# Optimization experiments

Hardware: AMD Instinct MI355X
Metric: run time of the kernel (lower is better)

Reference implementation:

```python
import jax, jax.numpy as jnp
import numpy as np

EPS = 1e-10
NUM_RELATION = 4
N_NODES = 50000
N_EDGES = 800000
D_IN = 128
D_H = 256


def rgc_layer(x, src, dst, rel, rel_w, rel_b, loop_w, loop_b):
    # torchdrug RelationalGraphConv: scatter-mean per (node, relation), then
    # linear over concatenated per-relation features + self-loop linear + relu.
    N, d = x.shape
    msg = x[src]                                      # [E, d] gather
    idx = dst * NUM_RELATION + rel                    # [E] bucket per (node, relation)
    num_seg = N * NUM_RELATION
    agg = jax.ops.segment_sum(msg, idx, num_segments=num_seg)            # [N*R, d]
    cnt = jax.ops.segment_sum(jnp.ones((msg.shape[0], 1), x.dtype), idx,
                              num_segments=num_seg)                       # [N*R, 1]
    update = (agg / (cnt + EPS)).reshape(N, NUM_RELATION * d)            # [N, R*d]
    out = update @ rel_w + rel_b + x @ loop_w + loop_b                   # [N, d_out]
    return jax.nn.relu(out)


def highway(x, hp_w, hp_b, ht_w, ht_b):
    proj = jax.nn.relu(x @ hp_w + hp_b)
    gate = jax.nn.sigmoid(x @ ht_w + ht_b)
    return gate * proj + (1.0 - gate) * x


def setup_inputs() -> dict:
    key = jax.random.key(0)
    ks = jax.random.split(key, 16)
    s = 0.02
    inp = {
        "x": jax.random.normal(ks[0], (N_NODES, D_IN), dtype=jnp.float32),
        "src": jax.random.randint(ks[1], (N_EDGES,), 0, N_NODES, dtype=jnp.int32),
        "dst": jax.random.randint(ks[2], (N_EDGES,), 0, N_NODES, dtype=jnp.int32),
        "rel": jax.random.randint(ks[3], (N_EDGES,), 0, NUM_RELATION, dtype=jnp.int32),
        # layer 1: RGC(128->256) + Highway(256)
        "rel_w1": jax.random.normal(ks[4], (NUM_RELATION * D_IN, D_H), dtype=jnp.float32) * s,
        "rel_b1": jnp.zeros((D_H,), jnp.float32),
        "loop_w1": jax.random.normal(ks[5], (D_IN, D_H), dtype=jnp.float32) * s,
        "loop_b1": jnp.zeros((D_H,), jnp.float32),
        "hp_w1": jax.random.normal(ks[6], (D_H, D_H), dtype=jnp.float32) * s,
        "hp_b1": jnp.zeros((D_H,), jnp.float32),
        "ht_w1": jax.random.normal(ks[7], (D_H, D_H), dtype=jnp.float32) * s,
        "ht_b1": jnp.full((D_H,), -2.0, jnp.float32),  # transform.bias.data.fill_(-2.0)
        # layer 2: RGC(256->256) + Highway(256)
        "rel_w2": jax.random.normal(ks[8], (NUM_RELATION * D_H, D_H), dtype=jnp.float32) * s,
        "rel_b2": jnp.zeros((D_H,), jnp.float32),
        "loop_w2": jax.random.normal(ks[9], (D_H, D_H), dtype=jnp.float32) * s,
        "loop_b2": jnp.zeros((D_H,), jnp.float32),
        "hp_w2": jax.random.normal(ks[10], (D_H, D_H), dtype=jnp.float32) * s,
        "hp_b2": jnp.zeros((D_H,), jnp.float32),
        "ht_w2": jax.random.normal(ks[11], (D_H, D_H), dtype=jnp.float32) * s,
        "ht_b2": jnp.full((D_H,), -2.0, jnp.float32),
    }
    return inp


def reference(x, src, dst, rel,
              rel_w1, rel_b1, loop_w1, loop_b1, hp_w1, hp_b1, ht_w1, ht_b1,
              rel_w2, rel_b2, loop_w2, loop_b2, hp_w2, hp_b2, ht_w2, ht_b2):
    h = rgc_layer(x, src, dst, rel, rel_w1, rel_b1, loop_w1, loop_b1)
    h = highway(h, hp_w1, hp_b1, ht_w1, ht_b1)
    h = rgc_layer(h, src, dst, rel, rel_w2, rel_b2, loop_w2, loop_b2)
    h = highway(h, hp_w2, hp_b2, ht_w2, ht_b2)
    return h  # node_feature, shape [N, 256]
```

## Files before the change

### kernel.cpp

```cpp
#include <hip/hip_runtime.h>

typedef __bf16 bf16_t;
typedef __bf16 bf16x8 __attribute__((ext_vector_type(8)));
typedef __bf16 bf16x4 __attribute__((ext_vector_type(4)));
typedef float f32x4 __attribute__((ext_vector_type(4)));

#define BM 128
#define BN 128
#define BK 64

__device__ __forceinline__ void gload_lds16(const void* g, void* s) {
    __builtin_amdgcn_global_load_lds(
        (const __attribute__((address_space(1))) unsigned int*)g,
        (__attribute__((address_space(3))) unsigned int*)s, 16, 0, 0);
}

__global__ __launch_bounds__(256) void gemm_k(
    const bf16_t* __restrict__ A, int lda, int M,
    const bf16_t* __restrict__ Bt, int K,
    const float* __restrict__ bias, int relu_flag,
    bf16_t* __restrict__ outb, int ldo, int ocol,
    int NTM, int NTN)
{
    __shared__ __align__(16) bf16_t As[BM * BK];
    __shared__ __align__(16) bf16_t Bs[BN * BK];

    const int L    = blockIdx.x;
    const int xcd  = L & 7;
    const int rest = L >> 3;
    const int nt   = rest % NTN;
    const int sup  = rest / NTN;
    const int mt   = sup * 8 + xcd;
    if (mt >= NTM) return;
    const int m0 = mt * BM;
    const int n0 = nt * BN;

    const int tid  = threadIdx.x;
    const int wave = tid >> 6, lane = tid & 63;
    const int wr   = wave >> 1, wc = wave & 1;
    const int lm   = lane & 15, quad = lane >> 4;

    const bf16_t* ag[4];
    const bf16_t* bg[4];
    #pragma unroll
    for (int j = 0; j < 4; j++) {
        int c    = wave * 256 + j * 64 + lane;
        int row  = c >> 3;
        int cc   = (c & 7) ^ (row & 7);
        int col  = cc << 3;
        int gm   = m0 + row; if (gm >= M) gm = M - 1;
        ag[j] = A  + (size_t)gm * lda + col;
        bg[j] = Bt + (size_t)(n0 + row) * K + col;
    }

    f32x4 acc[4][4] = {};

    for (int k0 = 0; k0 < K; k0 += BK) {
        __syncthreads();
        #pragma unroll
        for (int j = 0; j < 4; j++)
            gload_lds16(ag[j] + k0, As + (size_t)(wave * 256 + j * 64) * 8);
        #pragma unroll
        for (int j = 0; j < 4; j++)
            gload_lds16(bg[j] + k0, Bs + (size_t)(wave * 256 + j * 64) * 8);
        __syncthreads();

        #pragma unroll
        for (int h = 0; h < 2; h++) {
            bf16x8 af[4], bfr[4];
            #pragma unroll
            for (int i = 0; i < 4; i++) {
                int r = wr * 64 + i * 16 + lm;
                af[i] = *(const bf16x8*)&As[(size_t)(r * 8 + ((h * 4 + quad) ^ (r & 7))) * 8];
            }
            #pragma unroll
            for (int i = 0; i < 4; i++) {
                int r = wc * 64 + i * 16 + lm;
                bfr[i] = *(const bf16x8*)&Bs[(size_t)(r * 8 + ((h * 4 + quad) ^ (r & 7))) * 8];
            }
            #pragma unroll
            for (int mi = 0; mi < 4; mi++)
                #pragma unroll
                for (int ni = 0; ni < 4; ni++)
                    acc[mi][ni] = __builtin_amdgcn_mfma_f32_16x16x32_bf16(
                        af[mi], bfr[ni], acc[mi][ni], 0, 0, 0);
        }
    }

    #pragma unroll
    for (int mi = 0; mi < 4; mi++) {
        #pragma unroll
        for (int ni = 0; ni < 4; ni++) {
            int col = n0 + wc * 64 + ni * 16 + lm;
            float b = bias[col];
            #pragma unroll
            for (int r = 0; r < 4; r++) {
                int row = m0 + wr * 64 + mi * 16 + quad * 4 + r;
                if (row < M) {
                    float v = acc[mi][ni][r] + b;
                    if (relu_flag) v = fmaxf(v, 0.f);
                    outb[(size_t)row * ldo + ocol + col] = (bf16_t)v;
                }
            }
        }
    }
}

__global__ void count_k(const int* __restrict__ dst, const int* __restrict__ rel,
                        int* __restrict__ cnt, int E)
{
    int e = blockIdx.x * blockDim.x + threadIdx.x;
    if (e < E) atomicAdd(&cnt[dst[e] * 4 + rel[e]], 1);
}

__global__ void scan_partial(const int* __restrict__ cnt, int* __restrict__ offs,
                             int* __restrict__ chunkSums, int NSEG)
{
    __shared__ int sh[256];
    int t = threadIdx.x;
    int idx = blockIdx.x * 256 + t;
    int v = (idx < NSEG) ? cnt[idx] : 0;
    sh[t] = v;
    __syncthreads();
    for (int d = 1; d < 256; d <<= 1) {
        int add = (t >= d) ? sh[t - d] : 0;
        __syncthreads();
        sh[t] += add;
        __syncthreads();
    }
    if (idx < NSEG) offs[idx] = sh[t] - v;
    if (t == 255) chunkSums[blockIdx.x] = sh[t];
}

__global__ void scan_chunks(int* __restrict__ chunkSums, int NCHUNK)
{
    __shared__ int sh[1024];
    int t = threadIdx.x;
    int v = (t < NCHUNK) ? chunkSums[t] : 0;
    sh[t] = v;
    __syncthreads();
    for (int d = 1; d < 1024; d <<= 1) {
        int add = (t >= d) ? sh[t - d] : 0;
        __syncthreads();
        sh[t] += add;
        __syncthreads();
    }
    if (t < NCHUNK) chunkSums[t] = sh[t] - v;
}

__global__ void scan_add(int* __restrict__ offs, const int* __restrict__ chunkSums,
                         int* __restrict__ cursor, int NSEG)
{
    int idx = blockIdx.x * 256 + threadIdx.x;
    if (idx < NSEG) {
        int o = offs[idx] + chunkSums[blockIdx.x];
        offs[idx] = o;
        cursor[idx] = o;
    }
}

__global__ void fill_k(const int* __restrict__ src, const int* __restrict__ dst,
                       const int* __restrict__ rel,
                       int* __restrict__ cursor, int* __restrict__ eidx, int E)
{
    int e = blockIdx.x * blockDim.x + threadIdx.x;
    if (e < E) {
        int seg = dst[e] * 4 + rel[e];
        int pos = atomicAdd(&cursor[seg], 1);
        eidx[pos] = src[e];
    }
}

__global__ void seg_mean256(const int* __restrict__ offs, const int* __restrict__ cnt,
                            const int* __restrict__ eidx,
                            const bf16_t* __restrict__ xb, int ldx,
                            bf16_t* __restrict__ Aout, int lda, int NSEG)
{
    int wv = (blockIdx.x << 2) + (threadIdx.x >> 6);
    if (wv >= NSEG) return;
    int lane = threadIdx.x & 63;
    int c = lane << 2;
    int start = offs[wv];
    int n = cnt[wv];
    f32x4 acc = {};
    int i = 0;
    for (; i + 4 <= n; i += 4) {
        int s0 = eidx[start + i + 0];
        int s1 = eidx[start + i + 1];
        int s2 = eidx[start + i + 2];
        int s3 = eidx[start + i + 3];
        bf16x4 v0 = *(const bf16x4*)(xb + (size_t)s0 * ldx + c);
        bf16x4 v1 = *(const bf16x4*)(xb + (size_t)s1 * ldx + c);
        bf16x4 v2 = *(const bf16x4*)(xb + (size_t)s2 * ldx + c);
        bf16x4 v3 = *(const bf16x4*)(xb + (size_t)s3 * ldx + c);
        #pragma unroll
        for (int j = 0; j < 4; j++)
            acc[j] += ((float)v0[j] + (float)v1[j]) + ((float)v2[j] + (float)v3[j]);
    }
    for (; i < n; i++) {
        int s = eidx[start + i];
        bf16x4 v = *(const bf16x4*)(xb + (size_t)s * ldx + c);
        #pragma unroll
        for (int j = 0; j < 4; j++) acc[j] += (float)v[j];
    }
    float inv = 1.0f / ((float)n + 1e-10f);
    int node = wv >> 2, r = wv & 3;
    bf16x4 o;
    o[0] = (bf16_t)(acc[0] * inv);
    o[1] = (bf16_t)(acc[1] * inv);
    o[2] = (bf16_t)(acc[2] * inv);
    o[3] = (bf16_t)(acc[3] * inv);
    *(bf16x4*)(Aout + (size_t)node * lda + r * 256 + c) = o;
}

__global__ void seg_mean128(const int* __restrict__ offs, const int* __restrict__ cnt,
                            const int* __restrict__ eidx,
                            const bf16_t* __restrict__ xb, int ldx,
                            bf16_t* __restrict__ Aout, int lda, int NSEG)
{
    int wv = (blockIdx.x << 2) + (threadIdx.x >> 6);
    if (wv >= NSEG) return;
    int lane = threadIdx.x & 63;
    int half = lane >> 5;
    int c = (lane & 31) << 2;
    int start = offs[wv];
    int n = cnt[wv];
    f32x4 acc = {};
    int i = 0;
    for (; i + 4 <= n; i += 4) {
        int s0 = eidx[start + i + half];
        int s1 = eidx[start + i + 2 + half];
        bf16x4 v0 = *(const bf16x4*)(xb + (size_t)s0 * ldx + c);
        bf16x4 v1 = *(const bf16x4*)(xb + (size_t)s1 * ldx + c);
        #pragma unroll
        for (int j = 0; j < 4; j++) acc[j] += (float)v0[j] + (float)v1[j];
    }
    for (; i + 2 <= n; i += 2) {
        int s = eidx[start + i + half];
        bf16x4 v = *(const bf16x4*)(xb + (size_t)s * ldx + c);
        #pragma unroll
        for (int j = 0; j < 4; j++) acc[j] += (float)v[j];
    }
    if (i < n && half == 0) {
        int s = eidx[start + i];
        bf16x4 v = *(const bf16x4*)(xb + (size_t)s * ldx + c);
        #pragma unroll
        for (int j = 0; j < 4; j++) acc[j] += (float)v[j];
    }
    #pragma unroll
    for (int j = 0; j < 4; j++) acc[j] += __shfl_xor(acc[j], 32, 64);
    if (half == 0) {
        float inv = 1.0f / ((float)n + 1e-10f);
        int node = wv >> 2, r = wv & 3;
        bf16x4 o;
        o[0] = (bf16_t)(acc[0] * inv);
        o[1] = (bf16_t)(acc[1] * inv);
        o[2] = (bf16_t)(acc[2] * inv);
        o[3] = (bf16_t)(acc[3] * inv);
        *(bf16x4*)(Aout + (size_t)node * lda + r * 128 + c) = o;
    }
}

__global__ void convert_x_k(const float* __restrict__ x, bf16_t* __restrict__ A1, int N)
{
    int t = blockIdx.x * blockDim.x + threadIdx.x;
    if (t >= N * 32) return;
    int row = t >> 5;
    int c = (t & 31) << 2;
    f32x4 v = *(const f32x4*)(x + (size_t)row * 128 + c);
    bf16x4 o;
    o[0] = (bf16_t)v[0]; o[1] = (bf16_t)v[1]; o[2] = (bf16_t)v[2]; o[3] = (bf16_t)v[3];
    *(bf16x4*)(A1 + (size_t)row * 640 + 512 + c) = o;
}

__global__ void transpose_w(const float* __restrict__ W, bf16_t* __restrict__ Wt,
                            int K, int ldk, int k0, int n0)
{
    int t = blockIdx.x * blockDim.x + threadIdx.x;
    if (t >= K * 256) return;
    int k = t >> 8, n = t & 255;
    Wt[(size_t)(n0 + n) * ldk + k0 + k] = (bf16_t)W[(size_t)k * 256 + n];
}

__global__ void prep_bias(const float* rb1, const float* lb1,
                          const float* rb2, const float* lb2,
                          const float* hpb1, const float* htb1,
                          const float* hpb2, const float* htb2,
                          float* bR1, float* bR2, float* bH1, float* bH2)
{
    int t = threadIdx.x;
    bR1[t] = rb1[t] + lb1[t];
    bR2[t] = rb2[t] + lb2[t];
    bH1[t] = hpb1[t]; bH1[256 + t] = htb1[t];
    bH2[t] = hpb2[t]; bH2[256 + t] = htb2[t];
}

__global__ void highway_k(const bf16_t* __restrict__ PG, const bf16_t* __restrict__ h,
                          int N, bf16_t* __restrict__ outb, int ldo, int ocol,
                          float* __restrict__ outf)
{
    int t = blockIdx.x * blockDim.x + threadIdx.x;
    if (t >= N * 64) return;
    int row = t >> 6;
    int c = (t & 63) << 2;
    size_t ip = (size_t)row * 512 + c;
    bf16x4 p = *(const bf16x4*)(PG + ip);
    bf16x4 g = *(const bf16x4*)(PG + ip + 256);
    bf16x4 hv = *(const bf16x4*)(h + (size_t)row * 256 + c);
    bf16x4 ob;
    f32x4 of;
    #pragma unroll
    for (int j = 0; j < 4; j++) {
        float gg = 1.0f / (1.0f + __expf(-(float)g[j]));
        float pp = fmaxf((float)p[j], 0.f);
        float v = gg * pp + (1.0f - gg) * (float)hv[j];
        ob[j] = (bf16_t)v;
        of[j] = v;
    }
    if (outb) *(bf16x4*)(outb + (size_t)row * ldo + ocol + c) = ob;
    if (outf) *(f32x4*)(outf + (size_t)row * 256 + c) = of;
}

extern "C" void kernel_launch(void* const* d_in, const int* in_sizes, int n_in,
                              void* d_out, int out_size, void* d_ws, size_t ws_size,
                              hipStream_t stream)
{
    const float* x       = (const float*)d_in[0];
    const int*   src     = (const int*)d_in[1];
    const int*   dst     = (const int*)d_in[2];
    const int*   rel     = (const int*)d_in[3];
    const float* rel_w1  = (const float*)d_in[4];
    const float* rel_b1  = (const float*)d_in[5];
    const float* loop_w1 = (const float*)d_in[6];
    const float* loop_b1 = (const float*)d_in[7];
    const float* hp_w1   = (const float*)d_in[8];
    const float* hp_b1   = (const float*)d_in[9];
    const float* ht_w1   = (const float*)d_in[10];
    const float* ht_b1   = (const float*)d_in[11];
    const float* rel_w2  = (const float*)d_in[12];
    const float* rel_b2  = (const float*)d_in[13];
    const float* loop_w2 = (const float*)d_in[14];
    const float* loop_b2 = (const float*)d_in[15];
    const float* hp_w2   = (const float*)d_in[16];
    const float* hp_b2   = (const float*)d_in[17];
    const float* ht_w2   = (const float*)d_in[18];
    const float* ht_b2   = (const float*)d_in[19];

    const int N = in_sizes[0] / 128;
    const int E = in_sizes[1];
    const int NSEG = N * 4;
    const int NCHUNK = (NSEG + 255) / 256;
    float* out = (float*)d_out;

    char* ws = (char*)d_ws;
    size_t off = 0;
    auto alloc = [&](size_t bytes) {
        void* p = ws + off;
        off += (bytes + 255) & ~(size_t)255;
        return p;
    };
    int*    cnt    = (int*)alloc((size_t)NSEG * 4);
    int*    offs   = (int*)alloc((size_t)NSEG * 4);
    int*    cursor = (int*)alloc((size_t)NSEG * 4);
    int*    chunkS = (int*)alloc(4096);
    int*    eidx   = (int*)alloc((size_t)E * 4);
    bf16_t* A1     = (bf16_t*)alloc((size_t)N * 640 * 2);
    bf16_t* A2     = (bf16_t*)alloc((size_t)N * 1280 * 2);
    bf16_t* h      = (bf16_t*)alloc((size_t)N * 256 * 2);
    bf16_t* W1t    = (bf16_t*)alloc((size_t)256 * 640 * 2);
    bf16_t* W2t    = (bf16_t*)alloc((size_t)256 * 1280 * 2);
    bf16_t* Wh1t   = (bf16_t*)alloc((size_t)512 * 256 * 2);
    bf16_t* Wh2t   = (bf16_t*)alloc((size_t)512 * 256 * 2);
    float*  bR1    = (float*)alloc(256 * 4);
    float*  bR2    = (float*)alloc(256 * 4);
    float*  bH1    = (float*)alloc(512 * 4);
    float*  bH2    = (float*)alloc(512 * 4);
    bf16_t* PG     = A1;

    dim3 blk(256);
    const int NTM = (N + BM - 1) / BM;
    const int supers = (NTM + 7) / 8;
    const int gridRGC = supers * 8 * 2;
    const int gridHW  = supers * 8 * 4;

    transpose_w<<<dim3(512), blk, 0, stream>>>(rel_w1, W1t, 512, 640, 0, 0);
    transpose_w<<<dim3(128), blk, 0, stream>>>(loop_w1, W1t, 128, 640, 512, 0);
    transpose_w<<<dim3(1024), blk, 0, stream>>>(rel_w2, W2t, 1024, 1280, 0, 0);
    transpose_w<<<dim3(256), blk, 0, stream>>>(loop_w2, W2t, 256, 1280, 1024, 0);
    transpose_w<<<dim3(256), blk, 0, stream>>>(hp_w1, Wh1t, 256, 256, 0, 0);
    transpose_w<<<dim3(256), blk, 0, stream>>>(ht_w1, Wh1t, 256, 256, 0, 256);
    transpose_w<<<dim3(256), blk, 0, stream>>>(hp_w2, Wh2t, 256, 256, 0, 0);
    transpose_w<<<dim3(256), blk, 0, stream>>>(ht_w2, Wh2t, 256, 256, 0, 256);
    prep_bias<<<dim3(1), blk, 0, stream>>>(rel_b1, loop_b1, rel_b2, loop_b2,
                                           hp_b1, ht_b1, hp_b2, ht_b2,
                                           bR1, bR2, bH1, bH2);
    convert_x_k<<<dim3((N * 32 + 255) / 256), blk, 0, stream>>>(x, A1, N);

    hipMemsetAsync(cnt, 0, (size_t)NSEG * 4, stream);
    count_k<<<dim3((E + 255) / 256), blk, 0, stream>>>(dst, rel, cnt, E);
    scan_partial<<<dim3(NCHUNK), blk, 0, stream>>>(cnt, offs, chunkS, NSEG);
    scan_chunks<<<dim3(1), dim3(1024), 0, stream>>>(chunkS, NCHUNK);
    scan_add<<<dim3(NCHUNK), blk, 0, stream>>>(offs, chunkS, cursor, NSEG);
    fill_k<<<dim3((E + 255) / 256), blk, 0, stream>>>(src, dst, rel, cursor, eidx, E);

    seg_mean128<<<dim3((NSEG + 3) / 4), blk, 0, stream>>>(offs, cnt, eidx,
                                                          A1 + 512, 640, A1, 640, NSEG);
    gemm_k<<<dim3(gridRGC), blk, 0, stream>>>(A1, 640, N, W1t, 640,
                                              bR1, 1, h, 256, 0, NTM, 2);
    gemm_k<<<dim3(gridHW), blk, 0, stream>>>(h, 256, N, Wh1t, 256,
                                             bH1, 0, PG, 512, 0, NTM, 4);
    highway_k<<<dim3((N * 64 + 255) / 256), blk, 0, stream>>>(PG, h, N,
                                                              A2, 1280, 1024, nullptr);

    seg_mean256<<<dim3((NSEG + 3) / 4), blk, 0, stream>>>(offs, cnt, eidx,
                                                          A2 + 1024, 1280, A2, 1280, NSEG);
    gemm_k<<<dim3(gridRGC), blk, 0, stream>>>(A2, 1280, N, W2t, 1280,
                                              bR2, 1, h, 256, 0, NTM, 2);
    gemm_k<<<dim3(gridHW), blk, 0, stream>>>(h, 256, N, Wh2t, 256,
                                             bH2, 0, PG, 512, 0, NTM, 4);
    highway_k<<<dim3((N * 64 + 255) / 256), blk, 0, stream>>>(PG, h, N,
                                                              nullptr, 0, 0, out);
}
```

Before: 582.1 us.

## Fuse highway gate/proj GEMM with highway epilogue and widen segment-mean loads

```diff
diff --git a/kernel.cpp b/kernel.cpp
--- a/kernel.cpp
+++ b/kernel.cpp
@@ -106,6 +106,108 @@
     }
 }
 
+__global__ __launch_bounds__(256) void gemm_hw(
+    const bf16_t* __restrict__ A, int M,
+    const bf16_t* __restrict__ Bt,
+    const float* __restrict__ bias,
+    bf16_t* __restrict__ outb, int ldo, int ocol,
+    float* __restrict__ outf, int NTM)
+{
+    const int K = 256;
+    __shared__ __align__(16) bf16_t As[128 * 64];
+    __shared__ __align__(16) bf16_t Bs[2 * 128 * 64];
+
+    const int L    = blockIdx.x;
+    const int xcd  = L & 7;
+    const int rest = L >> 3;
+    const int nt   = rest % 2;
+    const int sup  = rest / 2;
+    const int mt   = sup * 8 + xcd;
+    if (mt >= NTM) return;
+    const int m0 = mt * 128;
+
+    const int tid  = threadIdx.x;
+    const int wave = tid >> 6, lane = tid & 63;
+    const int wr   = wave >> 1, wc = wave & 1;
+    const int lm   = lane & 15, quad = lane >> 4;
+
+    const bf16_t* ag[4];
+    const bf16_t* bg[4];
+    #pragma unroll
+    for (int j = 0; j < 4; j++) {
+        int c    = wave * 256 + j * 64 + lane;
+        int row  = c >> 3;
+        int cc   = (c & 7) ^ (row & 7);
+        int col  = cc << 3;
+        int gm   = m0 + row; if (gm >= M) gm = M - 1;
+        ag[j] = A  + (size_t)gm * 256 + col;
+        bg[j] = Bt + (size_t)(nt * 128 + row) * 256 + col;
+    }
+
+    f32x4 acc[4][8] = {};
+
+    for (int k0 = 0; k0 < K; k0 += 64) {
+        __syncthreads();
+        #pragma unroll
+        for (int j = 0; j < 4; j++)
+            gload_lds16(ag[j] + k0, As + (size_t)(wave * 256 + j * 64) * 8);
+        #pragma unroll
+        for (int j = 0; j < 4; j++)
+            gload_lds16(bg[j] + k0, Bs + (size_t)(wave * 256 + j * 64) * 8);
+        #pragma unroll
+        for (int j = 0; j < 4; j++)
+            gload_lds16(bg[j] + 65536 + k0,
+                        Bs + (size_t)(8192 + wave * 256 + j * 64) * 8);
+        __syncthreads();
+
+        #pragma unroll
+        for (int h = 0; h < 2; h++) {
+            bf16x8 af[4], bfr[8];
+            #pragma unroll
+            for (int i = 0; i < 4; i++) {
+                int r = wr * 64 + i * 16 + lm;
+                af[i] = *(const bf16x8*)&As[(size_t)(r * 8 + ((h * 4 + quad) ^ (r & 7))) * 8];
+            }
+            #pragma unroll
+            for (int i = 0; i < 8; i++) {
+                int strip = i >> 2;
+                int r = wc * 64 + (i & 3) * 16 + lm;
+                bfr[i] = *(const bf16x8*)&Bs[(size_t)(strip * 8192 + r * 8 +
+                                                      ((h * 4 + quad) ^ (r & 7))) * 8];
+            }
+            #pragma unroll
+            for (int mi = 0; mi < 4; mi++)
+                #pragma unroll
+                for (int ni = 0; ni < 8; ni++)
+                    acc[mi][ni] = __builtin_amdgcn_mfma_f32_16x16x32_bf16(
+                        af[mi], bfr[ni], acc[mi][ni], 0, 0, 0);
+        }
+    }
+
+    #pragma unroll
+    for (int mi = 0; mi < 4; mi++) {
+        #pragma unroll
+        for (int ni = 0; ni < 4; ni++) {
+            int cP = nt * 128 + wc * 64 + ni * 16 + lm;
+            float bp = bias[cP];
+            float bgc = bias[256 + cP];
+            #pragma unroll
+            for (int r = 0; r < 4; r++) {
+                int row = m0 + wr * 64 + mi * 16 + quad * 4 + r;
+                if (row < M) {
+                    float p = acc[mi][ni][r] + bp;
+                    float g = acc[mi][ni + 4][r] + bgc;
+                    float s = 1.0f / (1.0f + __expf(-g));
+                    float hv = (float)A[(size_t)row * 256 + cP];
+                    float v = s * fmaxf(p, 0.f) + (1.0f - s) * hv;
+                    if (outf) outf[(size_t)row * 256 + cP] = v;
+                    else      outb[(size_t)row * ldo + ocol + cP] = (bf16_t)v;
+                }
+            }
+        }
+    }
+}
+
 __global__ void count_k(const int* __restrict__ dst, const int* __restrict__ rel,
                         int* __restrict__ cnt, int E)
 {
@@ -179,38 +281,47 @@
     int wv = (blockIdx.x << 2) + (threadIdx.x >> 6);
     if (wv >= NSEG) return;
     int lane = threadIdx.x & 63;
-    int c = lane << 2;
+    int half = lane >> 5;
+    int c = (lane & 31) << 3;
     int start = offs[wv];
     int n = cnt[wv];
-    f32x4 acc = {};
+    float acc[8] = {};
     int i = 0;
-    for (; i + 4 <= n; i += 4) {
-        int s0 = eidx[start + i + 0];
-        int s1 = eidx[start + i + 1];
-        int s2 = eidx[start + i + 2];
-        int s3 = eidx[start + i + 3];
-        bf16x4 v0 = *(const bf16x4*)(xb + (size_t)s0 * ldx + c);
-        bf16x4 v1 = *(const bf16x4*)(xb + (size_t)s1 * ldx + c);
-        bf16x4 v2 = *(const bf16x4*)(xb + (size_t)s2 * ldx + c);
-        bf16x4 v3 = *(const bf16x4*)(xb + (size_t)s3 * ldx + c);
-        #pragma unroll
-        for (int j = 0; j < 4; j++)
+    for (; i + 8 <= n; i += 8) {
+        int s0 = eidx[start + i + 0 + half];
+        int s1 = eidx[start + i + 2 + half];
+        int s2 = eidx[start + i + 4 + half];
+        int s3 = eidx[start + i + 6 + half];
+        bf16x8 v0 = *(const bf16x8*)(xb + (size_t)s0 * ldx + c);
+        bf16x8 v1 = *(const bf16x8*)(xb + (size_t)s1 * ldx + c);
+        bf16x8 v2 = *(const bf16x8*)(xb + (size_t)s2 * ldx + c);
+        bf16x8 v3 = *(const bf16x8*)(xb + (size_t)s3 * ldx + c);
+        #pragma unroll
+        for (int j = 0; j < 8; j++)
             acc[j] += ((float)v0[j] + (float)v1[j]) + ((float)v2[j] + (float)v3[j]);
     }
-    for (; i < n; i++) {
+    for (; i + 2 <= n; i += 2) {
+        int s = eidx[start + i + half];
+        bf16x8 v = *(const bf16x8*)(xb + (size_t)s * ldx + c);
+        #pragma unroll
+        for (int j = 0; j < 8; j++) acc[j] += (float)v[j];
+    }
+    if (i < n && half == 0) {
         int s = eidx[start + i];
-        bf16x4 v = *(const bf16x4*)(xb + (size_t)s * ldx + c);
-        #pragma unroll
-        for (int j = 0; j < 4; j++) acc[j] += (float)v[j];
-    }
-    float inv = 1.0f / ((float)n + 1e-10f);
-    int node = wv >> 2, r = wv & 3;
-    bf16x4 o;
-    o[0] = (bf16_t)(acc[0] * inv);
-    o[1] = (bf16_t)(acc[1] * inv);
-    o[2] = (bf16_t)(acc[2] * inv);
-    o[3] = (bf16_t)(acc[3] * inv);
-    *(bf16x4*)(Aout + (size_t)node * lda + r * 256 + c) = o;
+        bf16x8 v = *(const bf16x8*)(xb + (size_t)s * ldx + c);
+        #pragma unroll
+        for (int j = 0; j < 8; j++) acc[j] += (float)v[j];
+    }
+    #pragma unroll
+    for (int j = 0; j < 8; j++) acc[j] += __shfl_xor(acc[j], 32, 64);
+    if (half == 0) {
+        float inv = 1.0f / ((float)n + 1e-10f);
+        int node = wv >> 2, r = wv & 3;
+        bf16x8 o;
+        #pragma unroll
+        for (int j = 0; j < 8; j++) o[j] = (bf16_t)(acc[j] * inv);
+        *(bf16x8*)(Aout + (size_t)node * lda + r * 256 + c) = o;
+    }
 }
 
 __global__ void seg_mean128(const int* __restrict__ offs, const int* __restrict__ cnt,
@@ -221,43 +332,44 @@
     int wv = (blockIdx.x << 2) + (threadIdx.x >> 6);
     if (wv >= NSEG) return;
     int lane = threadIdx.x & 63;
-    int half = lane >> 5;
-    int c = (lane & 31) << 2;
+    int q = lane >> 4;
+    int c = (lane & 15) << 3;
     int start = offs[wv];
     int n = cnt[wv];
-    f32x4 acc = {};
+    float acc[8] = {};
     int i = 0;
+    for (; i + 8 <= n; i += 8) {
+        int s0 = eidx[start + i + q];
+        int s1 = eidx[start + i + 4 + q];
+        bf16x8 v0 = *(const bf16x8*)(xb + (size_t)s0 * ldx + c);
+        bf16x8 v1 = *(const bf16x8*)(xb + (size_t)s1 * ldx + c);
+        #pragma unroll
+        for (int j = 0; j < 8; j++) acc[j] += (float)v0[j] + (float)v1[j];
+    }
     for (; i + 4 <= n; i += 4) {
-        int s0 = eidx[start + i + half];
-        int s1 = eidx[start + i + 2 + half];
-        bf16x4 v0 = *(const bf16x4*)(xb + (size_t)s0 * ldx + c);
-        bf16x4 v1 = *(const bf16x4*)(xb + (size_t)s1 * ldx + c);
-        #pragma unroll
-        for (int j = 0; j < 4; j++) acc[j] += (float)v0[j] + (float)v1[j];
-    }
-    for (; i + 2 <= n; i += 2) {
-        int s = eidx[start + i + half];
-        bf16x4 v = *(const bf16x4*)(xb + (size_t)s * ldx + c);
-        #pragma unroll
-        for (int j = 0; j < 4; j++) acc[j] += (float)v[j];
-    }
-    if (i < n && half == 0) {
-        int s = eidx[start + i];
-        bf16x4 v = *(const bf16x4*)(xb + (size_t)s * ldx + c);
-        #pragma unroll
-        for (int j = 0; j < 4; j++) acc[j] += (float)v[j];
+        int s = eidx[start + i + q];
+        bf16x8 v = *(const bf16x8*)(xb + (size_t)s * ldx + c);
+        #pragma unroll
+        for (int j = 0; j < 8; j++) acc[j] += (float)v[j];
+    }
+    if (q < n - i) {
+        int s = eidx[start + i + q];
+        bf16x8 v = *(const bf16x8*)(xb + (size_t)s * ldx + c);
+        #pragma unroll
+        for (int j = 0; j < 8; j++) acc[j] += (float)v[j];
     }
     #pragma unroll
-    for (int j = 0; j < 4; j++) acc[j] += __shfl_xor(acc[j], 32, 64);
-    if (half == 0) {
+    for (int j = 0; j < 8; j++) {
+        acc[j] += __shfl_xor(acc[j], 16, 64);
+        acc[j] += __shfl_xor(acc[j], 32, 64);
+    }
+    if (lane < 16) {
         float inv = 1.0f / ((float)n + 1e-10f);
         int node = wv >> 2, r = wv & 3;
-        bf16x4 o;
-        o[0] = (bf16_t)(acc[0] * inv);
-        o[1] = (bf16_t)(acc[1] * inv);
-        o[2] = (bf16_t)(acc[2] * inv);
-        o[3] = (bf16_t)(acc[3] * inv);
-        *(bf16x4*)(Aout + (size_t)node * lda + r * 128 + c) = o;
+        bf16x8 o;
+        #pragma unroll
+        for (int j = 0; j < 8; j++) o[j] = (bf16_t)(acc[j] * inv);
+        *(bf16x8*)(Aout + (size_t)node * lda + r * 128 + c) = o;
     }
 }
 
@@ -293,32 +405,6 @@
     bR2[t] = rb2[t] + lb2[t];
     bH1[t] = hpb1[t]; bH1[256 + t] = htb1[t];
     bH2[t] = hpb2[t]; bH2[256 + t] = htb2[t];
-}
-
-__global__ void highway_k(const bf16_t* __restrict__ PG, const bf16_t* __restrict__ h,
-                          int N, bf16_t* __restrict__ outb, int ldo, int ocol,
-                          float* __restrict__ outf)
-{
-    int t = blockIdx.x * blockDim.x + threadIdx.x;
-    if (t >= N * 64) return;
-    int row = t >> 6;
-    int c = (t & 63) << 2;
-    size_t ip = (size_t)row * 512 + c;
-    bf16x4 p = *(const bf16x4*)(PG + ip);
-    bf16x4 g = *(const bf16x4*)(PG + ip + 256);
-    bf16x4 hv = *(const bf16x4*)(h + (size_t)row * 256 + c);
-    bf16x4 ob;
-    f32x4 of;
-    #pragma unroll
-    for (int j = 0; j < 4; j++) {
-        float gg = 1.0f / (1.0f + __expf(-(float)g[j]));
-        float pp = fmaxf((float)p[j], 0.f);
-        float v = gg * pp + (1.0f - gg) * (float)hv[j];
-        ob[j] = (bf16_t)v;
-        of[j] = v;
-    }
-    if (outb) *(bf16x4*)(outb + (size_t)row * ldo + ocol + c) = ob;
-    if (outf) *(f32x4*)(outf + (size_t)row * 256 + c) = of;
 }
 
 extern "C" void kernel_launch(void* const* d_in, const int* in_sizes, int n_in,
@@ -375,13 +461,12 @@
     float*  bR2    = (float*)alloc(256 * 4);
     float*  bH1    = (float*)alloc(512 * 4);
     float*  bH2    = (float*)alloc(512 * 4);
-    bf16_t* PG     = A1;
 
     dim3 blk(256);
     const int NTM = (N + BM - 1) / BM;
     const int supers = (NTM + 7) / 8;
     const int gridRGC = supers * 8 * 2;
-    const int gridHW  = supers * 8 * 4;
+    const int gridHW  = supers * 8 * 2;
 
     transpose_w<<<dim3(512), blk, 0, stream>>>(rel_w1, W1t, 512, 640, 0, 0);
     transpose_w<<<dim3(128), blk, 0, stream>>>(loop_w1, W1t, 128, 640, 512, 0);
@@ -407,17 +492,13 @@
                                                           A1 + 512, 640, A1, 640, NSEG);
     gemm_k<<<dim3(gridRGC), blk, 0, stream>>>(A1, 640, N, W1t, 640,
                                               bR1, 1, h, 256, 0, NTM, 2);
-    gemm_k<<<dim3(gridHW), blk, 0, stream>>>(h, 256, N, Wh1t, 256,
-                                             bH1, 0, PG, 512, 0, NTM, 4);
-    highway_k<<<dim3((N * 64 + 255) / 256), blk, 0, stream>>>(PG, h, N,
-                                                              A2, 1280, 1024, nullptr);
+    gemm_hw<<<dim3(gridHW), blk, 0, stream>>>(h, N, Wh1t, bH1,
+                                              A2, 1280, 1024, nullptr, NTM);
 
     seg_mean256<<<dim3((NSEG + 3) / 4), blk, 0, stream>>>(offs, cnt, eidx,
                                                           A2 + 1024, 1280, A2, 1280, NSEG);
     gemm_k<<<dim3(gridRGC), blk, 0, stream>>>(A2, 1280, N, W2t, 1280,
                                               bR2, 1, h, 256, 0, NTM, 2);
-    gemm_k<<<dim3(gridHW), blk, 0, stream>>>(h, 256, N, Wh2t, 256,
-                                             bH2, 0, PG, 512, 0, NTM, 4);
-    highway_k<<<dim3((N * 64 + 255) / 256), blk, 0, stream>>>(PG, h, N,
-                                                              nullptr, 0, 0, out);
-}
+    gemm_hw<<<dim3(gridHW), blk, 0, stream>>>(h, N, Wh2t, bH2,
+                                              nullptr, 0, 0, out, NTM);
+}
```

After: 619.7 us. +6.5%, slower.
